# Kernel tuning notes

Measured on AMD Instinct MI355X. Metric: run time of the kernel, lower is better.

## Reference

```python
import jax, jax.numpy as jnp
import numpy as np

TEMPERATURE = 0.07
B, D = 8192, 256

def _l2norm(x, axis=-1, eps=1e-12):
    # matches torch F.normalize(p=2): x / max(||x||, eps)
    n = jnp.sqrt(jnp.sum(x * x, axis=axis, keepdims=True))
    return x / jnp.maximum(n, eps)

def setup_inputs() -> dict:
    key = jax.random.key(0)
    k1, k2, k3 = jax.random.split(key, 3)
    return {
        "h_emb": jax.random.normal(k1, (B, D), dtype=jnp.float32),
        "r_emb": jax.random.normal(k2, (B, D), dtype=jnp.float32),
        "t_emb": jax.random.normal(k3, (B, D), dtype=jnp.float32),
    }

def reference(h_emb, r_emb, t_emb):
    # query = normalize(h + r); positives/negatives = normalize(t)
    q = _l2norm(h_emb + r_emb, axis=1)          # [B, D]
    t = _l2norm(t_emb, axis=1)                  # [B, D]
    # Dense in-batch similarity. The original builds logits = [pos, off-diag negs];
    # since the diagonal of sim IS the positive similarity, cross-entropy with
    # label 0 equals logsumexp over the full row minus the diagonal entry.
    sim = jnp.einsum('bd,nd->bn', q, t) / TEMPERATURE   # [B, B]
    pos = jnp.diagonal(sim)                              # [B]
    loss = jnp.mean(jax.nn.logsumexp(sim, axis=1) - pos)
    return loss
```

## Files before the change

kernel.cpp:

```cpp
#include <hip/hip_runtime.h>
#include <hip/hip_bf16.h>

#define B_DIM 8192
#define D_DIM 256
#define GRID_GEMM 512
#define NT 16

constexpr float INV_T = 14.285714285714286f;

typedef __bf16 bf16x8 __attribute__((ext_vector_type(8)));
typedef float  f32x16 __attribute__((ext_vector_type(16)));

#define GLOBAL_U32(p) ((const __attribute__((address_space(1))) unsigned int*)(p))
#define LDS_U32(p)    ((__attribute__((address_space(3))) unsigned int*)(p))

#define WAITCNT_VM8 0x0F78

__device__ inline unsigned short f2bf(float f) {
    union { float f; unsigned u; } x; x.f = f;
    unsigned r = x.u + 0x7fffu + ((x.u >> 16) & 1u);
    return (unsigned short)(r >> 16);
}

__global__ __launch_bounds__(256) void norm_kernel(
    const float* __restrict__ h, const float* __restrict__ r,
    const float* __restrict__ t,
    unsigned short* __restrict__ qws, unsigned short* __restrict__ tws,
    float* __restrict__ rowsum, float* __restrict__ diagsum, int* __restrict__ ticket)
{
    if (blockIdx.x == 0) {
        float4* rs4 = (float4*)rowsum;
#pragma unroll
        for (int i = 0; i < 8; ++i)
            rs4[threadIdx.x * 8 + i] = make_float4(0.f, 0.f, 0.f, 0.f);
        if (threadIdx.x == 0) { *diagsum = 0.f; *ticket = 0; }
    }

    const int wave = threadIdx.x >> 6;
    const int lane = threadIdx.x & 63;
    const int wg   = blockIdx.x * 4 + wave;

    const int ks  = lane >> 2;
    const int hi2 = (lane >> 1) & 1;
    const int sub = lane & 1;

#pragma unroll
    for (int i = 0; i < 2; ++i) {
        const int row = wg * 2 + i;
        {
            float4 a = ((const float4*)h)[row * 64 + lane];
            float4 b = ((const float4*)r)[row * 64 + lane];
            float4 v = make_float4(a.x + b.x, a.y + b.y, a.z + b.z, a.w + b.w);
            float s = v.x * v.x + v.y * v.y + v.z * v.z + v.w * v.w;
#pragma unroll
            for (int off = 32; off; off >>= 1) s += __shfl_xor(s, off, 64);
            float scale = 1.0f / fmaxf(sqrtf(s), 1e-12f);
            ushort4 o;
            o.x = f2bf(v.x * scale); o.y = f2bf(v.y * scale);
            o.z = f2bf(v.z * scale); o.w = f2bf(v.w * scale);
            size_t slot16 = ((size_t)((row >> 5) * 16 + ks) * 64
                             + (size_t)(hi2 * 32 + (row & 31)));
            *(ushort4*)((unsigned char*)qws + slot16 * 16 + sub * 8) = o;
        }
        {
            float4 v = ((const float4*)t)[row * 64 + lane];
            float s = v.x * v.x + v.y * v.y + v.z * v.z + v.w * v.w;
#pragma unroll
            for (int off = 32; off; off >>= 1) s += __shfl_xor(s, off, 64);
            float scale = 1.0f / fmaxf(sqrtf(s), 1e-12f);
            ushort4 o;
            o.x = f2bf(v.x * scale); o.y = f2bf(v.y * scale);
            o.z = f2bf(v.z * scale); o.w = f2bf(v.w * scale);
            size_t slot16 = ((size_t)((row >> 5) * 16 + ks) * 64
                             + (size_t)(hi2 * 32 + (row & 31)));
            *(ushort4*)((unsigned char*)tws + slot16 * 16 + sub * 8) = o;
        }
    }
}

__global__ __launch_bounds__(256, 2) void gemm_lse_kernel(
    const unsigned char* __restrict__ qws, const unsigned char* __restrict__ tws,
    float* __restrict__ rowsum, float* __restrict__ diagsum,
    int* __restrict__ ticket, float* __restrict__ out)
{
    __shared__ __align__(16) unsigned char ldsB[4][32 * 512];
    __shared__ float wred[4];
    __shared__ int lastflag;

    const int tid  = threadIdx.x;
    const int lane = tid & 63;
    const int w    = tid >> 6;
    const int l31  = lane & 31;
    const int hi   = lane >> 5;

    const int cc   = blockIdx.x & 15;
    const int rb   = blockIdx.x >> 4;
    const int row0 = rb * 256 + w * 64;
    const int col0 = cc * 512;
    const int tile0 = cc * 16;

#define STAGE(snt, bufi)                                                     \
    {                                                                        \
        const unsigned char* gs = tws + (size_t)(tile0 + (snt)) * 16384;     \
        _Pragma("unroll")                                                    \
        for (int it = 0; it < 4; ++it)                                       \
            __builtin_amdgcn_global_load_lds(                                \
                GLOBAL_U32(gs + (it * 256 + tid) * 16),                      \
                LDS_U32(&ldsB[bufi][(it * 256 + tid) * 16]), 16, 0, 0);      \
    }

    STAGE(0, 0);
    STAGE(1, 1);

    bf16x8 a[2][16];
    {
        const unsigned char* abase = qws + (size_t)row0 * 512 + lane * 16;
#pragma unroll
        for (int rt = 0; rt < 2; ++rt)
#pragma unroll
            for (int ks = 0; ks < 16; ++ks)
                a[rt][ks] = *(const bf16x8*)(abase + rt * 16384 + ks * 1024);
    }

    f32x16 rowacc[2] = {};
    float diagacc = 0.f;

    for (int nt = 0; nt < NT; ++nt) {
        const int snt = (nt + 2 < NT) ? nt + 2 : NT - 1;
        STAGE(snt, (nt + 2) & 3);

        __builtin_amdgcn_s_waitcnt(WAITCNT_VM8);
        __builtin_amdgcn_s_barrier();

        const unsigned char* bbuf = ldsB[nt & 3] + lane * 16;
        f32x16 acc0 = {}, acc1 = {};
#pragma unroll
        for (int ks = 0; ks < 16; ++ks) {
            bf16x8 b = *(const bf16x8*)(bbuf + ks * 1024);
            acc0 = __builtin_amdgcn_mfma_f32_32x32x16_bf16(a[0][ks], b, acc0, 0, 0, 0);
            acc1 = __builtin_amdgcn_mfma_f32_32x32x16_bf16(a[1][ks], b, acc1, 0, 0, 0);
        }

#pragma unroll
        for (int g = 0; g < 16; ++g) {
            rowacc[0][g] += __expf(fmaf(acc0[g], INV_T, -INV_T));
            rowacc[1][g] += __expf(fmaf(acc1[g], INV_T, -INV_T));
        }

        const int c0t = col0 + nt * 32;
        if (c0t == row0) {
#pragma unroll
            for (int g = 0; g < 16; ++g) {
                int rm = (g & 3) + 8 * (g >> 2) + 4 * hi;
                if (l31 == rm) diagacc += acc0[g] * INV_T;
            }
        }
        if (c0t == row0 + 32) {
#pragma unroll
            for (int g = 0; g < 16; ++g) {
                int rm = (g & 3) + 8 * (g >> 2) + 4 * hi;
                if (l31 == rm) diagacc += acc1[g] * INV_T;
            }
        }
    }

#pragma unroll
    for (int rt = 0; rt < 2; ++rt)
#pragma unroll
        for (int g = 0; g < 16; ++g) {
            float s = rowacc[rt][g];
            s += __shfl_xor(s, 1, 64);
            s += __shfl_xor(s, 2, 64);
            s += __shfl_xor(s, 4, 64);
            s += __shfl_xor(s, 8, 64);
            s += __shfl_xor(s, 16, 64);
            if (l31 == 0) {
                int grow = row0 + rt * 32 + (g & 3) + 8 * (g >> 2) + 4 * hi;
                atomicAdd(&rowsum[grow], s);
            }
        }

    float dsum = diagacc;
#pragma unroll
    for (int off = 32; off; off >>= 1) dsum += __shfl_xor(dsum, off, 64);
    if (lane == 0 && dsum != 0.f) atomicAdd(diagsum, dsum);

    __syncthreads();
    if (tid == 0) {
        __threadfence();
        int old = __hip_atomic_fetch_add(ticket, 1, __ATOMIC_ACQ_REL,
                                         __HIP_MEMORY_SCOPE_AGENT);
        lastflag = (old == GRID_GEMM - 1);
    }
    __syncthreads();
    if (!lastflag) return;

    float lsum = 0.f;
    for (int rr = tid; rr < B_DIM; rr += 256) {
        float rs = __hip_atomic_load(&rowsum[rr], __ATOMIC_RELAXED,
                                     __HIP_MEMORY_SCOPE_AGENT);
        lsum += __logf(rs);
    }
#pragma unroll
    for (int off = 32; off; off >>= 1) lsum += __shfl_xor(lsum, off, 64);
    if (lane == 0) wred[w] = lsum;
    __syncthreads();
    if (tid == 0) {
        float ds = __hip_atomic_load(diagsum, __ATOMIC_RELAXED,
                                     __HIP_MEMORY_SCOPE_AGENT);
        float total = wred[0] + wred[1] + wred[2] + wred[3]
                    + (float)B_DIM * INV_T
                    - ds;
        out[0] = total / (float)B_DIM;
    }
}

extern "C" void kernel_launch(void* const* d_in, const int* in_sizes, int n_in,
                              void* d_out, int out_size, void* d_ws, size_t ws_size,
                              hipStream_t stream)
{
    const float* h = (const float*)d_in[0];
    const float* r = (const float*)d_in[1];
    const float* t = (const float*)d_in[2];

    unsigned char* ws = (unsigned char*)d_ws;
    unsigned short* qws = (unsigned short*)ws;
    unsigned short* tws = (unsigned short*)(ws + 4u * 1024 * 1024);
    float* rowsum  = (float*)(ws + 8u * 1024 * 1024);
    float* diagsum = (float*)(ws + 8u * 1024 * 1024 + 32u * 1024);
    int*   ticket  = (int*)  (ws + 8u * 1024 * 1024 + 32u * 1024 + 16);

    norm_kernel<<<1024, 256, 0, stream>>>(h, r, t, qws, tws, rowsum, diagsum, ticket);
    gemm_lse_kernel<<<GRID_GEMM, 256, 0, stream>>>(
        (const unsigned char*)qws, (const unsigned char*)tws,
        rowsum, diagsum, ticket, (float*)d_out);
}
```

Measured before the change: 132.4 us.

## Double GEMM grid and split B tiles into K-halves for finer pipelining

The grid doubles to 1024 blocks, so each block covers 256 columns (8 column tiles) instead of 512. Each 32-column tile is staged as two 8 KB K-half subtiles in a 4-deep LDS ring, and the wait count is adjusted to match. The goal is more blocks for occupancy and load balance and a smaller LDS footprint per block. In exchange there are twice as many barriers per tile, each block reloads its A rows, and twice as many rowsum atomics are issued.

```diff
diff --git a/kernel.cpp b/kernel.cpp
--- a/kernel.cpp
+++ b/kernel.cpp
@@ -3,8 +3,9 @@
 
 #define B_DIM 8192
 #define D_DIM 256
-#define GRID_GEMM 512
-#define NT 16
+#define GRID_GEMM 1024
+#define NCT 8
+#define NSUB 16
 
 constexpr float INV_T = 14.285714285714286f;
 
@@ -14,7 +15,7 @@
 #define GLOBAL_U32(p) ((const __attribute__((address_space(1))) unsigned int*)(p))
 #define LDS_U32(p)    ((__attribute__((address_space(3))) unsigned int*)(p))
 
-#define WAITCNT_VM8 0x0F78
+#define WAITCNT_VM4 0x0F74
 
 __device__ inline unsigned short f2bf(float f) {
     union { float f; unsigned u; } x; x.f = f;
@@ -83,7 +84,7 @@
     float* __restrict__ rowsum, float* __restrict__ diagsum,
     int* __restrict__ ticket, float* __restrict__ out)
 {
-    __shared__ __align__(16) unsigned char ldsB[4][32 * 512];
+    __shared__ __align__(16) unsigned char ldsB[4][8192];
     __shared__ float wred[4];
     __shared__ int lastflag;
 
@@ -93,17 +94,17 @@
     const int l31  = lane & 31;
     const int hi   = lane >> 5;
 
-    const int cc   = blockIdx.x & 15;
-    const int rb   = blockIdx.x >> 4;
+    const int cc   = blockIdx.x & 31;
+    const int rb   = blockIdx.x >> 5;
     const int row0 = rb * 256 + w * 64;
-    const int col0 = cc * 512;
-    const int tile0 = cc * 16;
-
-#define STAGE(snt, bufi)                                                     \
+    const int col0 = cc * 256;
+    const int subt0 = cc * 16;
+
+#define STAGE(s, bufi)                                                       \
     {                                                                        \
-        const unsigned char* gs = tws + (size_t)(tile0 + (snt)) * 16384;     \
+        const unsigned char* gs = tws + (size_t)(subt0 + (s)) * 8192;        \
         _Pragma("unroll")                                                    \
-        for (int it = 0; it < 4; ++it)                                       \
+        for (int it = 0; it < 2; ++it)                                       \
             __builtin_amdgcn_global_load_lds(                                \
                 GLOBAL_U32(gs + (it * 256 + tid) * 16),                      \
                 LDS_U32(&ldsB[bufi][(it * 256 + tid) * 16]), 16, 0, 0);      \
@@ -125,20 +126,26 @@
     f32x16 rowacc[2] = {};
     float diagacc = 0.f;
 
-    for (int nt = 0; nt < NT; ++nt) {
-        const int snt = (nt + 2 < NT) ? nt + 2 : NT - 1;
-        STAGE(snt, (nt + 2) & 3);
-
-        __builtin_amdgcn_s_waitcnt(WAITCNT_VM8);
-        __builtin_amdgcn_s_barrier();
-
-        const unsigned char* bbuf = ldsB[nt & 3] + lane * 16;
+    for (int ct = 0; ct < NCT; ++ct) {
         f32x16 acc0 = {}, acc1 = {};
 #pragma unroll
-        for (int ks = 0; ks < 16; ++ks) {
-            bf16x8 b = *(const bf16x8*)(bbuf + ks * 1024);
-            acc0 = __builtin_amdgcn_mfma_f32_32x32x16_bf16(a[0][ks], b, acc0, 0, 0, 0);
-            acc1 = __builtin_amdgcn_mfma_f32_32x32x16_bf16(a[1][ks], b, acc1, 0, 0, 0);
+        for (int kh = 0; kh < 2; ++kh) {
+            const int s = ct * 2 + kh;
+            const int sn = (s + 2 < NSUB) ? s + 2 : NSUB - 1;
+            STAGE(sn, (s + 2) & 3);
+
+            __builtin_amdgcn_s_waitcnt(WAITCNT_VM4);
+            __builtin_amdgcn_s_barrier();
+
+            const unsigned char* bbuf = ldsB[s & 3] + lane * 16;
+#pragma unroll
+            for (int ks = 0; ks < 8; ++ks) {
+                bf16x8 b = *(const bf16x8*)(bbuf + ks * 1024);
+                acc0 = __builtin_amdgcn_mfma_f32_32x32x16_bf16(
+                           a[0][kh * 8 + ks], b, acc0, 0, 0, 0);
+                acc1 = __builtin_amdgcn_mfma_f32_32x32x16_bf16(
+                           a[1][kh * 8 + ks], b, acc1, 0, 0, 0);
+            }
         }
 
 #pragma unroll
@@ -147,7 +154,7 @@
             rowacc[1][g] += __expf(fmaf(acc1[g], INV_T, -INV_T));
         }
 
-        const int c0t = col0 + nt * 32;
+        const int c0t = col0 + ct * 32;
         if (c0t == row0) {
 #pragma unroll
             for (int g = 0; g < 16; ++g) {
```

After: 153.6 us. +16.0%, slower.

## Process two B tiles per barrier and fold temperature into query normalization

Applied to the files above, without the earlier changes.

The GEMM main loop now handles two 32-column tiles per iteration. Each iteration waits for all outstanding loads, issues a barrier, prefetches the next two tiles into the 4-slot LDS ring, then runs both MFMA tiles. This halves the number of barrier and waitcnt points and gives each prefetch two tiles of compute to hide behind. The 1/T scale is now applied when normalizing q, so the epilogue does a subtraction before exp instead of an fma, and the diagonal needs no multiply. The cost is bf16 quantization of a pre-scaled q, and a full vmcnt(0) wait that leaves no loads in flight across the barrier.

```diff
diff --git a/kernel.cpp b/kernel.cpp
--- a/kernel.cpp
+++ b/kernel.cpp
@@ -14,7 +14,7 @@
 #define GLOBAL_U32(p) ((const __attribute__((address_space(1))) unsigned int*)(p))
 #define LDS_U32(p)    ((__attribute__((address_space(3))) unsigned int*)(p))
 
-#define WAITCNT_VM8 0x0F78
+#define WAITCNT_VM0 0x0F70
 
 __device__ inline unsigned short f2bf(float f) {
     union { float f; unsigned u; } x; x.f = f;
@@ -54,7 +54,7 @@
             float s = v.x * v.x + v.y * v.y + v.z * v.z + v.w * v.w;
 #pragma unroll
             for (int off = 32; off; off >>= 1) s += __shfl_xor(s, off, 64);
-            float scale = 1.0f / fmaxf(sqrtf(s), 1e-12f);
+            float scale = INV_T / fmaxf(sqrtf(s), 1e-12f);
             ushort4 o;
             o.x = f2bf(v.x * scale); o.y = f2bf(v.y * scale);
             o.z = f2bf(v.z * scale); o.w = f2bf(v.w * scale);
@@ -99,9 +99,9 @@
     const int col0 = cc * 512;
     const int tile0 = cc * 16;
 
-#define STAGE(snt, bufi)                                                     \
+#define STAGE(st, bufi)                                                      \
     {                                                                        \
-        const unsigned char* gs = tws + (size_t)(tile0 + (snt)) * 16384;     \
+        const unsigned char* gs = tws + (size_t)(tile0 + (st)) * 16384;      \
         _Pragma("unroll")                                                    \
         for (int it = 0; it < 4; ++it)                                       \
             __builtin_amdgcn_global_load_lds(                                \
@@ -125,43 +125,47 @@
     f32x16 rowacc[2] = {};
     float diagacc = 0.f;
 
-    for (int nt = 0; nt < NT; ++nt) {
-        const int snt = (nt + 2 < NT) ? nt + 2 : NT - 1;
-        STAGE(snt, (nt + 2) & 3);
-
-        __builtin_amdgcn_s_waitcnt(WAITCNT_VM8);
+#define PROCESS_TILE(t)                                                      \
+    {                                                                        \
+        const unsigned char* bbuf = ldsB[(t) & 3] + lane * 16;               \
+        f32x16 acc0 = {}, acc1 = {};                                         \
+        _Pragma("unroll")                                                    \
+        for (int ks = 0; ks < 16; ++ks) {                                    \
+            bf16x8 b = *(const bf16x8*)(bbuf + ks * 1024);                   \
+            acc0 = __builtin_amdgcn_mfma_f32_32x32x16_bf16(a[0][ks], b, acc0, 0, 0, 0); \
+            acc1 = __builtin_amdgcn_mfma_f32_32x32x16_bf16(a[1][ks], b, acc1, 0, 0, 0); \
+        }                                                                    \
+        _Pragma("unroll")                                                    \
+        for (int g = 0; g < 16; ++g) {                                       \
+            rowacc[0][g] += __expf(acc0[g] - INV_T);                         \
+            rowacc[1][g] += __expf(acc1[g] - INV_T);                         \
+        }                                                                    \
+        const int c0t = col0 + (t) * 32;                                     \
+        if (c0t == row0) {                                                   \
+            _Pragma("unroll")                                                \
+            for (int g = 0; g < 16; ++g) {                                   \
+                int rm = (g & 3) + 8 * (g >> 2) + 4 * hi;                    \
+                if (l31 == rm) diagacc += acc0[g];                           \
+            }                                                                \
+        }                                                                    \
+        if (c0t == row0 + 32) {                                              \
+            _Pragma("unroll")                                                \
+            for (int g = 0; g < 16; ++g) {                                   \
+                int rm = (g & 3) + 8 * (g >> 2) + 4 * hi;                    \
+                if (l31 == rm) diagacc += acc1[g];                           \
+            }                                                                \
+        }                                                                    \
+    }
+
+    for (int r = 0; r < 8; ++r) {
+        __builtin_amdgcn_s_waitcnt(WAITCNT_VM0);
         __builtin_amdgcn_s_barrier();
-
-        const unsigned char* bbuf = ldsB[nt & 3] + lane * 16;
-        f32x16 acc0 = {}, acc1 = {};
-#pragma unroll
-        for (int ks = 0; ks < 16; ++ks) {
-            bf16x8 b = *(const bf16x8*)(bbuf + ks * 1024);
-            acc0 = __builtin_amdgcn_mfma_f32_32x32x16_bf16(a[0][ks], b, acc0, 0, 0, 0);
-            acc1 = __builtin_amdgcn_mfma_f32_32x32x16_bf16(a[1][ks], b, acc1, 0, 0, 0);
-        }
-
-#pragma unroll
-        for (int g = 0; g < 16; ++g) {
-            rowacc[0][g] += __expf(fmaf(acc0[g], INV_T, -INV_T));
-            rowacc[1][g] += __expf(fmaf(acc1[g], INV_T, -INV_T));
-        }
-
-        const int c0t = col0 + nt * 32;
-        if (c0t == row0) {
-#pragma unroll
-            for (int g = 0; g < 16; ++g) {
-                int rm = (g & 3) + 8 * (g >> 2) + 4 * hi;
-                if (l31 == rm) diagacc += acc0[g] * INV_T;
-            }
-        }
-        if (c0t == row0 + 32) {
-#pragma unroll
-            for (int g = 0; g < 16; ++g) {
-                int rm = (g & 3) + 8 * (g >> 2) + 4 * hi;
-                if (l31 == rm) diagacc += acc1[g] * INV_T;
-            }
-        }
+        if (r < 7) {
+            STAGE(2 * r + 2, (2 * r + 2) & 3);
+            STAGE(2 * r + 3, (2 * r + 3) & 3);
+        }
+        PROCESS_TILE(2 * r);
+        PROCESS_TILE(2 * r + 1);
     }
 
 #pragma unroll
```

New measurement: 132.0 us. No clear change (-0.3%).
